# Optimization experiments

Measured on AMD Instinct MI355X. Metric: run time of the kernel, lower is better.

Reference implementation:

```python
import jax, jax.numpy as jnp
import numpy as np

ROWS, COLS, NFEAT = 128, 128, 256
BATCH = 4096


def setup_inputs() -> dict:
    key = jax.random.key(0)
    k1, k2 = jax.random.split(key)
    xb = jax.random.normal(k1, (BATCH, NFEAT), dtype=jnp.float32)
    weights = jax.random.normal(k2, (ROWS, COLS, NFEAT), dtype=jnp.float32)
    return {"xb": xb, "weights": weights}


def reference(xb, weights):
    # Flatten codebook: (M, F) with M = rows*cols
    w = weights.reshape(-1, NFEAT)
    # Pairwise Euclidean distances via ||a||^2 + ||b||^2 - 2 a.b (single GEMM)
    a2 = jnp.sum(xb * xb, axis=-1, keepdims=True)            # (B, 1)
    b2 = jnp.sum(w * w, axis=-1)                             # (M,)
    d2 = a2 + b2[None, :] - 2.0 * jnp.einsum('bf,mf->bm', xb, w)  # (B, M)
    distances = jnp.sqrt(jnp.maximum(d2, 0.0))
    # BMU: argmin over codebook, converted to 2D map indices
    min_idxs = jnp.argmin(distances, axis=-1)                # (B,)
    bmus = jnp.stack([min_idxs // COLS, min_idxs % COLS], axis=-1)  # (B, 2)
    return bmus
```

## Files before the change

kernel.cpp:

```cpp
#include <hip/hip_runtime.h>
#include <cfloat>

#define NFEAT 256
#define BATCH 4096
#define MTOT  16384
#define NSTRIP 8
#define STRIPW 2048
#define NHALF 32
#define UMARGIN 0.75f

typedef __attribute__((ext_vector_type(8))) short bf16x8;
typedef __attribute__((ext_vector_type(4))) float f32x4;

#define GP(p)    ((const __attribute__((address_space(1))) void*)(p))
#define LDSP(p)  ((__attribute__((address_space(3))) void*)(p))

__device__ __forceinline__ unsigned bf16pack(float a, float b) {
    unsigned ua = __float_as_uint(a), ub = __float_as_uint(b);
    unsigned ra = (ua + 0x7fffu + ((ua >> 16) & 1u)) >> 16;
    unsigned rb = (ub + 0x7fffu + ((ub >> 16) & 1u)) >> 16;
    return ra | (rb << 16);
}

__global__ __launch_bounds__(256) void prep_kernel(const float* __restrict__ xb,
                                                   const float* __restrict__ w,
                                                   uint2* __restrict__ Abf,
                                                   uint2* __restrict__ Bbf,
                                                   float* __restrict__ a2,
                                                   float* __restrict__ b2) {
    int gid  = blockIdx.x * blockDim.x + threadIdx.x;
    int row  = gid >> 6;
    int lane = gid & 63;
    const float* src;
    uint2* dst;
    float* nrm;
    if (row < MTOT) {
        src = w + (size_t)row * NFEAT;  dst = Bbf + (size_t)row * 64;  nrm = b2 + row;
    } else {
        int r = row - MTOT;
        src = xb + (size_t)r * NFEAT;   dst = Abf + (size_t)r * 64;    nrm = a2 + r;
    }
    float4 v = ((const float4*)src)[lane];
    dst[lane] = make_uint2(bf16pack(v.x, v.y), bf16pack(v.z, v.w));
    float s = v.x * v.x + v.y * v.y + v.z * v.z + v.w * v.w;
    #pragma unroll
    for (int off = 32; off > 0; off >>= 1) s += __shfl_down(s, off);
    if (lane == 0) *nrm = s;
}

__global__ __launch_bounds__(512, 1) void som_mfma_kernel(
        const unsigned short* __restrict__ Abf, const unsigned short* __restrict__ Bbf,
        const float* __restrict__ b2, float* __restrict__ part) {
    __shared__ char smem[139264];

    const int t = threadIdx.x, l = t & 63;
    const int wid = t >> 6, wm = wid >> 1, wc = wid & 1;
    const int strip = blockIdx.x & 7;
    const int m0 = (blockIdx.x >> 3) * 128;
    const int ns0 = strip * STRIPW;

    const int rowt = t >> 5;
    const int swzcol = ((t & 31) << 4) ^ ((rowt & 7) << 4);
    const char* gA = (const char*)Abf + (size_t)(m0 + rowt) * 512 + swzcol;
    const char* gB = (const char*)Bbf + (size_t)(ns0 + rowt) * 512 + swzcol;

    #pragma unroll
    for (int i = 0; i < 8; ++i)
        __builtin_amdgcn_global_load_lds(GP(gA + i * 8192), LDSP(smem + t * 16 + i * 8192), 16, 0, 0);
    __builtin_amdgcn_global_load_lds(GP((const char*)b2 + (size_t)ns0 * 4 + t * 16),
                                     LDSP(smem + 131072 + t * 16), 16, 0, 0);
    #pragma unroll
    for (int i = 0; i < 4; ++i)
        __builtin_amdgcn_global_load_lds(GP(gB + i * 8192), LDSP(smem + 65536 + t * 16 + i * 8192), 16, 0, 0);
    #pragma unroll
    for (int i = 0; i < 4; ++i)
        __builtin_amdgcn_global_load_lds(GP(gB + 32768 + i * 8192), LDSP(smem + 98304 + t * 16 + i * 8192), 16, 0, 0);

    float r0[2][4], r1[2][4];
    #pragma unroll
    for (int m = 0; m < 2; ++m)
        #pragma unroll
        for (int j = 0; j < 4; ++j) { r0[m][j] = -FLT_MAX; r1[m][j] = -FLT_MAX; }

    for (int h = 0; h < NHALF; ++h) {
        if (h < NHALF - 2) asm volatile("s_waitcnt vmcnt(4)" ::: "memory");
        else               asm volatile("s_waitcnt vmcnt(0)" ::: "memory");
        __builtin_amdgcn_s_barrier();
        asm volatile("" ::: "memory");

        const char* bufB = smem + 65536 + ((h & 1) << 15);
        const int cl = h * 64 + wc * 32 + (l & 15);
        const float b20 = -0.5f * *(const float*)(smem + 131072 + cl * 4);
        const float b21 = -0.5f * *(const float*)(smem + 131072 + cl * 4 + 64);

        f32x4 acc[2][2];
        #pragma unroll
        for (int m = 0; m < 2; ++m) {
            acc[m][0] = (f32x4){b20, b20, b20, b20};
            acc[m][1] = (f32x4){b21, b21, b21, b21};
        }

        #pragma unroll
        for (int kk = 0; kk < 8; ++kk) {
            const int swz = (kk * 64 + (l >> 4) * 16) ^ ((l & 7) << 4);
            bf16x8 af0 = *(const bf16x8*)(smem + (wm * 32 + (l & 15)) * 512 + swz);
            bf16x8 af1 = *(const bf16x8*)(smem + (wm * 32 + 16 + (l & 15)) * 512 + swz);
            bf16x8 bf0 = *(const bf16x8*)(bufB + (wc * 32 + (l & 15)) * 512 + swz);
            bf16x8 bf1 = *(const bf16x8*)(bufB + (wc * 32 + 16 + (l & 15)) * 512 + swz);
            acc[0][0] = __builtin_amdgcn_mfma_f32_16x16x32_bf16(af0, bf0, acc[0][0], 0, 0, 0);
            acc[0][1] = __builtin_amdgcn_mfma_f32_16x16x32_bf16(af0, bf1, acc[0][1], 0, 0, 0);
            acc[1][0] = __builtin_amdgcn_mfma_f32_16x16x32_bf16(af1, bf0, acc[1][0], 0, 0, 0);
            acc[1][1] = __builtin_amdgcn_mfma_f32_16x16x32_bf16(af1, bf1, acc[1][1], 0, 0, 0);
        }

        #pragma unroll
        for (int n = 0; n < 2; ++n) {
            const unsigned idn = (unsigned)(h * 2 + n);
            #pragma unroll
            for (int m = 0; m < 2; ++m)
                #pragma unroll
                for (int j = 0; j < 4; ++j) {
                    float p = __uint_as_float((__float_as_uint(acc[m][n][j]) & 0xFFFFFFC0u) | idn);
                    float nr1 = __builtin_amdgcn_fmed3f(r0[m][j], r1[m][j], p);
                    r0[m][j] = fmaxf(r0[m][j], p);
                    r1[m][j] = nr1;
                }
        }

        asm volatile("" ::: "memory");
        __builtin_amdgcn_s_barrier();
        asm volatile("" ::: "memory");
        if (h + 2 < NHALF) {
            const char* gBn = gB + (size_t)(h + 2) * 32768;
            const int dstb = 65536 + ((h & 1) << 15);
            #pragma unroll
            for (int i = 0; i < 4; ++i)
                __builtin_amdgcn_global_load_lds(GP(gBn + i * 8192),
                                                 LDSP(smem + dstb + t * 16 + i * 8192), 16, 0, 0);
        }
    }

    asm volatile("" ::: "memory");
    __builtin_amdgcn_s_barrier();
    asm volatile("" ::: "memory");
    float* sm = (float*)smem;
    #pragma unroll
    for (int m = 0; m < 2; ++m)
        #pragma unroll
        for (int j = 0; j < 4; ++j) {
            unsigned u0 = __float_as_uint(r0[m][j]);
            unsigned u1 = __float_as_uint(r1[m][j]);
            u0 = (u0 & 0xFFFFF800u) | ((u0 & 63u) << 5) | ((unsigned)wc << 4) | (unsigned)(l & 15);
            u1 = (u1 & 0xFFFFF800u) | ((u1 & 63u) << 5) | ((unsigned)wc << 4) | (unsigned)(l & 15);
            float v0 = __uint_as_float(u0), v1 = __uint_as_float(u1);
            #pragma unroll
            for (int off = 1; off < 16; off <<= 1) {
                float o0 = __shfl_xor(v0, off), o1 = __shfl_xor(v1, off);
                float nv1 = fmaxf(fminf(v0, o0), fmaxf(v1, o1));
                v0 = fmaxf(v0, o0);
                v1 = nv1;
            }
            if ((l & 15) == 0) {
                int row_l = wm * 32 + m * 16 + (l >> 4) * 4 + j;
                sm[row_l * 4 + wc * 2 + 0] = v0;
                sm[row_l * 4 + wc * 2 + 1] = v1;
            }
        }
    asm volatile("" ::: "memory");
    __builtin_amdgcn_s_barrier();
    asm volatile("" ::: "memory");
    if (t < 128) {
        float a0 = sm[t * 4 + 0], a1 = sm[t * 4 + 1];
        float c0 = sm[t * 4 + 2], c1 = sm[t * 4 + 3];
        float v0 = fmaxf(a0, c0);
        float v1 = fmaxf(fminf(a0, c0), fmaxf(a1, c1));
        float2* pp = (float2*)(part + ((size_t)(m0 + t) * NSTRIP + strip) * 2);
        *pp = make_float2(v0, v1);
    }
}

__global__ __launch_bounds__(256) void refine_kernel(
        const float* __restrict__ xb, const float* __restrict__ w,
        const float* __restrict__ a2, const float* __restrict__ b2,
        const float* __restrict__ part, int* __restrict__ out) {
    const int t = threadIdx.x, l = t & 63;
    const int row = blockIdx.x * 4 + (t >> 6);

    const float* pr = part + (size_t)row * (NSTRIP * 2);
    float v = (l < NSTRIP * 2) ? pr[l] : -FLT_MAX;
    float mx = v;
    #pragma unroll
    for (int off = 1; off < 64; off <<= 1) mx = fmaxf(mx, __shfl_xor(mx, off));
    const float cut = mx - UMARGIN;

    unsigned long long key = ~0ull;
    if (l < NSTRIP * 2 && v >= cut) {
        unsigned b = __float_as_uint(v);
        int lane4 = b & 15, wcb = (b >> 4) & 1, hn = (b >> 5) & 63;
        int col = (l >> 1) * STRIPW + (hn >> 1) * 64 + wcb * 32 + (hn & 1) * 16 + lane4;
        const float4* xr = (const float4*)(xb + (size_t)row * NFEAT);
        const float4* wr = (const float4*)(w + (size_t)col * NFEAT);
        float s0 = 0.f, s1 = 0.f, s2 = 0.f, s3 = 0.f;
        #pragma unroll
        for (int k = 0; k < 16; ++k) {
            float4 x0 = xr[4 * k + 0], w0 = wr[4 * k + 0];
            float4 x1 = xr[4 * k + 1], w1 = wr[4 * k + 1];
            float4 x2 = xr[4 * k + 2], w2 = wr[4 * k + 2];
            float4 x3 = xr[4 * k + 3], w3 = wr[4 * k + 3];
            s0 += x0.x * w0.x + x0.y * w0.y + x0.z * w0.z + x0.w * w0.w;
            s1 += x1.x * w1.x + x1.y * w1.y + x1.z * w1.z + x1.w * w1.w;
            s2 += x2.x * w2.x + x2.y * w2.y + x2.z * w2.z + x2.w * w2.w;
            s3 += x3.x * w3.x + x3.y * w3.y + x3.z * w3.z + x3.w * w3.w;
        }
        float dot = (s0 + s1) + (s2 + s3);
        float dd = a2[row] + b2[col] - 2.f * dot;
        float s = sqrtf(fmaxf(dd, 0.f));
        key = ((unsigned long long)__float_as_uint(s) << 32) | (unsigned)col;
    }
    #pragma unroll
    for (int off = 1; off < 64; off <<= 1) {
        unsigned long long o = __shfl_xor(key, off);
        key = o < key ? o : key;
    }
    if (l == 0) {
        int idx = (int)(key & 0xffffffffu);
        out[2 * row]     = idx >> 7;
        out[2 * row + 1] = idx & 127;
    }
}

extern "C" void kernel_launch(void* const* d_in, const int* in_sizes, int n_in,
                              void* d_out, int out_size, void* d_ws, size_t ws_size,
                              hipStream_t stream) {
    const float* xb = (const float*)d_in[0];
    const float* w  = (const float*)d_in[1];
    int* out = (int*)d_out;

    char* ws = (char*)d_ws;
    unsigned short* Abf = (unsigned short*)ws;
    unsigned short* Bbf = (unsigned short*)(ws + (2u << 20));
    float* a2   = (float*)(ws + (10u << 20));
    float* b2   = (float*)(ws + (10u << 20) + (64u << 10));
    float* part = (float*)(ws + (10u << 20) + (128u << 10));

    prep_kernel<<<((MTOT + BATCH) * 64) / 256, 256, 0, stream>>>(xb, w, (uint2*)Abf,
                                                                 (uint2*)Bbf, a2, b2);
    som_mfma_kernel<<<256, 512, 0, stream>>>(Abf, Bbf, b2, part);
    refine_kernel<<<BATCH / 4, 256, 0, stream>>>(xb, w, a2, b2, part, out);
}
```

Before: 85.26 us.

## Keep A fragments in registers and widen B tiles to 128 columns

Each wave now loads its 64-row slice of A straight from global memory into registers once, instead of staging A in LDS. LDS is used only for double-buffered 128-column B tiles over 16 iterations, with waves arranged 2x4. Each wave computes 4x2 MFMA tiles per step, which raises MFMA work per LDS read. The packed index bits in the top-2 tracker are rearranged for the new layout. Launch bounds ask for 2 blocks per CU, but the 139 KB LDS allocation and the large register use for A fragments may still limit occupancy to one block.

Measured after the change: 75.99 us. 10.9% less time.

```diff
diff --git a/kernel.cpp b/kernel.cpp
--- a/kernel.cpp
+++ b/kernel.cpp
@@ -6,14 +6,14 @@
 #define MTOT  16384
 #define NSTRIP 8
 #define STRIPW 2048
-#define NHALF 32
+#define NH 16
 #define UMARGIN 0.75f
 
 typedef __attribute__((ext_vector_type(8))) short bf16x8;
 typedef __attribute__((ext_vector_type(4))) float f32x4;
 
-#define GP(p)    ((const __attribute__((address_space(1))) void*)(p))
-#define LDSP(p)  ((__attribute__((address_space(3))) void*)(p))
+#define GP(p)   ((const __attribute__((address_space(1))) void*)(p))
+#define LDSP(p) ((__attribute__((address_space(3))) void*)(p))
 
 __device__ __forceinline__ unsigned bf16pack(float a, float b) {
     unsigned ua = __float_as_uint(a), ub = __float_as_uint(b);
@@ -48,54 +48,63 @@
     if (lane == 0) *nrm = s;
 }
 
-__global__ __launch_bounds__(512, 1) void som_mfma_kernel(
+__global__ __launch_bounds__(512, 2) void som_mfma_kernel(
         const unsigned short* __restrict__ Abf, const unsigned short* __restrict__ Bbf,
         const float* __restrict__ b2, float* __restrict__ part) {
     __shared__ char smem[139264];
 
     const int t = threadIdx.x, l = t & 63;
-    const int wid = t >> 6, wm = wid >> 1, wc = wid & 1;
+    const int wid = t >> 6;
+    const int wm = wid >> 2;
+    const int wc = wid & 3;
     const int strip = blockIdx.x & 7;
     const int m0 = (blockIdx.x >> 3) * 128;
     const int ns0 = strip * STRIPW;
 
     const int rowt = t >> 5;
     const int swzcol = ((t & 31) << 4) ^ ((rowt & 7) << 4);
-    const char* gA = (const char*)Abf + (size_t)(m0 + rowt) * 512 + swzcol;
     const char* gB = (const char*)Bbf + (size_t)(ns0 + rowt) * 512 + swzcol;
 
-    #pragma unroll
-    for (int i = 0; i < 8; ++i)
-        __builtin_amdgcn_global_load_lds(GP(gA + i * 8192), LDSP(smem + t * 16 + i * 8192), 16, 0, 0);
     __builtin_amdgcn_global_load_lds(GP((const char*)b2 + (size_t)ns0 * 4 + t * 16),
                                      LDSP(smem + 131072 + t * 16), 16, 0, 0);
     #pragma unroll
-    for (int i = 0; i < 4; ++i)
-        __builtin_amdgcn_global_load_lds(GP(gB + i * 8192), LDSP(smem + 65536 + t * 16 + i * 8192), 16, 0, 0);
-    #pragma unroll
-    for (int i = 0; i < 4; ++i)
-        __builtin_amdgcn_global_load_lds(GP(gB + 32768 + i * 8192), LDSP(smem + 98304 + t * 16 + i * 8192), 16, 0, 0);
-
-    float r0[2][4], r1[2][4];
-    #pragma unroll
-    for (int m = 0; m < 2; ++m)
+    for (int i = 0; i < 8; ++i)
+        __builtin_amdgcn_global_load_lds(GP(gB + i * 8192),
+                                         LDSP(smem + t * 16 + i * 8192), 16, 0, 0);
+    #pragma unroll
+    for (int i = 0; i < 8; ++i)
+        __builtin_amdgcn_global_load_lds(GP(gB + 65536 + i * 8192),
+                                         LDSP(smem + 65536 + t * 16 + i * 8192), 16, 0, 0);
+
+    const char* gA = (const char*)Abf
+                   + (size_t)(m0 + wm * 64 + (l & 15)) * 512 + (l >> 4) * 16;
+    bf16x8 afr[4][8];
+    #pragma unroll
+    for (int m = 0; m < 4; ++m)
+        #pragma unroll
+        for (int kk = 0; kk < 8; ++kk)
+            afr[m][kk] = *(const bf16x8*)(gA + (size_t)m * 16 * 512 + kk * 64);
+
+    float r0[4][4], r1[4][4];
+    #pragma unroll
+    for (int m = 0; m < 4; ++m)
         #pragma unroll
         for (int j = 0; j < 4; ++j) { r0[m][j] = -FLT_MAX; r1[m][j] = -FLT_MAX; }
 
-    for (int h = 0; h < NHALF; ++h) {
-        if (h < NHALF - 2) asm volatile("s_waitcnt vmcnt(4)" ::: "memory");
-        else               asm volatile("s_waitcnt vmcnt(0)" ::: "memory");
+    for (int h = 0; h < NH; ++h) {
+        if (h < NH - 1) asm volatile("s_waitcnt vmcnt(8)" ::: "memory");
+        else            asm volatile("s_waitcnt vmcnt(0)" ::: "memory");
         __builtin_amdgcn_s_barrier();
         asm volatile("" ::: "memory");
 
-        const char* bufB = smem + 65536 + ((h & 1) << 15);
-        const int cl = h * 64 + wc * 32 + (l & 15);
-        const float b20 = -0.5f * *(const float*)(smem + 131072 + cl * 4);
-        const float b21 = -0.5f * *(const float*)(smem + 131072 + cl * 4 + 64);
-
-        f32x4 acc[2][2];
-        #pragma unroll
-        for (int m = 0; m < 2; ++m) {
+        const char* bufB = smem + ((h & 1) << 16);
+        const int c0 = h * 128 + wc * 32 + (l & 15);
+        const float b20 = -0.5f * *(const float*)(smem + 131072 + c0 * 4);
+        const float b21 = -0.5f * *(const float*)(smem + 131072 + c0 * 4 + 64);
+
+        f32x4 acc[4][2];
+        #pragma unroll
+        for (int m = 0; m < 4; ++m) {
             acc[m][0] = (f32x4){b20, b20, b20, b20};
             acc[m][1] = (f32x4){b21, b21, b21, b21};
         }
@@ -103,24 +112,23 @@
         #pragma unroll
         for (int kk = 0; kk < 8; ++kk) {
             const int swz = (kk * 64 + (l >> 4) * 16) ^ ((l & 7) << 4);
-            bf16x8 af0 = *(const bf16x8*)(smem + (wm * 32 + (l & 15)) * 512 + swz);
-            bf16x8 af1 = *(const bf16x8*)(smem + (wm * 32 + 16 + (l & 15)) * 512 + swz);
             bf16x8 bf0 = *(const bf16x8*)(bufB + (wc * 32 + (l & 15)) * 512 + swz);
             bf16x8 bf1 = *(const bf16x8*)(bufB + (wc * 32 + 16 + (l & 15)) * 512 + swz);
-            acc[0][0] = __builtin_amdgcn_mfma_f32_16x16x32_bf16(af0, bf0, acc[0][0], 0, 0, 0);
-            acc[0][1] = __builtin_amdgcn_mfma_f32_16x16x32_bf16(af0, bf1, acc[0][1], 0, 0, 0);
-            acc[1][0] = __builtin_amdgcn_mfma_f32_16x16x32_bf16(af1, bf0, acc[1][0], 0, 0, 0);
-            acc[1][1] = __builtin_amdgcn_mfma_f32_16x16x32_bf16(af1, bf1, acc[1][1], 0, 0, 0);
+            #pragma unroll
+            for (int m = 0; m < 4; ++m) {
+                acc[m][0] = __builtin_amdgcn_mfma_f32_16x16x32_bf16(afr[m][kk], bf0, acc[m][0], 0, 0, 0);
+                acc[m][1] = __builtin_amdgcn_mfma_f32_16x16x32_bf16(afr[m][kk], bf1, acc[m][1], 0, 0, 0);
+            }
         }
 
         #pragma unroll
         for (int n = 0; n < 2; ++n) {
             const unsigned idn = (unsigned)(h * 2 + n);
             #pragma unroll
-            for (int m = 0; m < 2; ++m)
+            for (int m = 0; m < 4; ++m)
                 #pragma unroll
                 for (int j = 0; j < 4; ++j) {
-                    float p = __uint_as_float((__float_as_uint(acc[m][n][j]) & 0xFFFFFFC0u) | idn);
+                    float p = __uint_as_float((__float_as_uint(acc[m][n][j]) & 0xFFFFFFE0u) | idn);
                     float nr1 = __builtin_amdgcn_fmed3f(r0[m][j], r1[m][j], p);
                     r0[m][j] = fmaxf(r0[m][j], p);
                     r1[m][j] = nr1;
@@ -130,28 +138,25 @@
         asm volatile("" ::: "memory");
         __builtin_amdgcn_s_barrier();
         asm volatile("" ::: "memory");
-        if (h + 2 < NHALF) {
-            const char* gBn = gB + (size_t)(h + 2) * 32768;
-            const int dstb = 65536 + ((h & 1) << 15);
-            #pragma unroll
-            for (int i = 0; i < 4; ++i)
+        if (h + 2 < NH) {
+            const char* gBn = gB + (size_t)(h + 2) * 65536;
+            char* dst = smem + ((h & 1) << 16) + t * 16;
+            #pragma unroll
+            for (int i = 0; i < 8; ++i)
                 __builtin_amdgcn_global_load_lds(GP(gBn + i * 8192),
-                                                 LDSP(smem + dstb + t * 16 + i * 8192), 16, 0, 0);
-        }
-    }
-
-    asm volatile("" ::: "memory");
-    __builtin_amdgcn_s_barrier();
-    asm volatile("" ::: "memory");
+                                                 LDSP(dst + i * 8192), 16, 0, 0);
+        }
+    }
+
     float* sm = (float*)smem;
     #pragma unroll
-    for (int m = 0; m < 2; ++m)
+    for (int m = 0; m < 4; ++m)
         #pragma unroll
         for (int j = 0; j < 4; ++j) {
             unsigned u0 = __float_as_uint(r0[m][j]);
             unsigned u1 = __float_as_uint(r1[m][j]);
-            u0 = (u0 & 0xFFFFF800u) | ((u0 & 63u) << 5) | ((unsigned)wc << 4) | (unsigned)(l & 15);
-            u1 = (u1 & 0xFFFFF800u) | ((u1 & 63u) << 5) | ((unsigned)wc << 4) | (unsigned)(l & 15);
+            u0 = (u0 & 0xFFFFF800u) | ((u0 & 31u) << 6) | ((unsigned)wc << 4) | (unsigned)(l & 15);
+            u1 = (u1 & 0xFFFFF800u) | ((u1 & 31u) << 6) | ((unsigned)wc << 4) | (unsigned)(l & 15);
             float v0 = __uint_as_float(u0), v1 = __uint_as_float(u1);
             #pragma unroll
             for (int off = 1; off < 16; off <<= 1) {
@@ -161,21 +166,22 @@
                 v1 = nv1;
             }
             if ((l & 15) == 0) {
-                int row_l = wm * 32 + m * 16 + (l >> 4) * 4 + j;
-                sm[row_l * 4 + wc * 2 + 0] = v0;
-                sm[row_l * 4 + wc * 2 + 1] = v1;
+                int row_l = wm * 64 + m * 16 + (l >> 4) * 4 + j;
+                sm[row_l * 8 + wc * 2 + 0] = v0;
+                sm[row_l * 8 + wc * 2 + 1] = v1;
             }
         }
-    asm volatile("" ::: "memory");
-    __builtin_amdgcn_s_barrier();
-    asm volatile("" ::: "memory");
+    __syncthreads();
     if (t < 128) {
-        float a0 = sm[t * 4 + 0], a1 = sm[t * 4 + 1];
-        float c0 = sm[t * 4 + 2], c1 = sm[t * 4 + 3];
-        float v0 = fmaxf(a0, c0);
-        float v1 = fmaxf(fminf(a0, c0), fmaxf(a1, c1));
-        float2* pp = (float2*)(part + ((size_t)(m0 + t) * NSTRIP + strip) * 2);
-        *pp = make_float2(v0, v1);
+        float V0 = -FLT_MAX, V1 = -FLT_MAX;
+        #pragma unroll
+        for (int q = 0; q < 4; ++q) {
+            float a0 = sm[t * 8 + q * 2], a1 = sm[t * 8 + q * 2 + 1];
+            float nv1 = fmaxf(fminf(V0, a0), fmaxf(V1, a1));
+            V0 = fmaxf(V0, a0);
+            V1 = nv1;
+        }
+        ((float2*)part)[(size_t)(m0 + t) * NSTRIP + strip] = make_float2(V0, V1);
     }
 }
 
@@ -196,8 +202,9 @@
     unsigned long long key = ~0ull;
     if (l < NSTRIP * 2 && v >= cut) {
         unsigned b = __float_as_uint(v);
-        int lane4 = b & 15, wcb = (b >> 4) & 1, hn = (b >> 5) & 63;
-        int col = (l >> 1) * STRIPW + (hn >> 1) * 64 + wcb * 32 + (hn & 1) * 16 + lane4;
+        int lane4 = b & 15, wcb = (b >> 4) & 3, inner = (b >> 6) & 31;
+        int col = (l >> 1) * STRIPW + (inner >> 1) * 128 + wcb * 32
+                + (inner & 1) * 16 + lane4;
         const float4* xr = (const float4*)(xb + (size_t)row * NFEAT);
         const float4* wr = (const float4*)(w + (size_t)col * NFEAT);
         float s0 = 0.f, s1 = 0.f, s2 = 0.f, s3 = 0.f;
```
